# Kernel optimization log

Hardware: AMD Instinct MI355X
Metric: run time of the kernel (lower is better)

Reference implementation:

```python
import jax, jax.numpy as jnp
import numpy as np

SEQ_LEN = 8192
D_K = 128
NEG_BIG = 1000000000.0


def setup_inputs() -> dict:
    key = jax.random.key(0)
    kq, kk, kv = jax.random.split(key, 3)
    q = jax.random.normal(kq, (SEQ_LEN, D_K), dtype=jnp.float32)
    k = jax.random.normal(kk, (SEQ_LEN, D_K), dtype=jnp.float32)
    v = jax.random.normal(kv, (SEQ_LEN, D_K), dtype=jnp.float32)
    return {"q": q, "k": k, "v": v}


def reference(q, k, v):
    # q,k,v: (S, d). Naive attention with causal (look-ahead) mask, masked=True.
    d_k = q.shape[-1]
    scaled_logits = jnp.matmul(q, k.T) / jnp.sqrt(jnp.asarray(d_k, q.dtype))  # (S, S)
    look_ahead_mask = jnp.triu(jnp.ones((SEQ_LEN, SEQ_LEN), dtype=q.dtype), k=1)
    scaled_logits = scaled_logits - look_ahead_mask * NEG_BIG
    attn = jnp.matmul(jax.nn.softmax(scaled_logits, axis=-1), v)  # (S, d)
    return attn
```

## Files before the change

kernel.cpp:

```cpp
#include <hip/hip_runtime.h>
#include <hip/hip_bf16.h>
#include <math.h>

#define S_LEN 8192
#define DK    128
#define BM    128
#define BN    64
#define NQT   (S_LEN / BM)
#define SCALE2 (0.08838834764831845f * 1.4426950408889634f)

typedef __bf16 bf16x8_t __attribute__((ext_vector_type(8)));
typedef __bf16 bf16x4_t __attribute__((ext_vector_type(4)));
typedef __bf16 bf16x2_t __attribute__((ext_vector_type(2)));
typedef float  floatx16 __attribute__((ext_vector_type(16)));
typedef unsigned uintx4 __attribute__((ext_vector_type(4)));

#define GLD16(g, l) __builtin_amdgcn_global_load_lds(                      \
    (const __attribute__((address_space(1))) void*)(g),                    \
    (__attribute__((address_space(3))) void*)(l), 16, 0, 0)

__device__ __forceinline__ float fexp2(float x) {
#if __has_builtin(__builtin_amdgcn_exp2f)
  return __builtin_amdgcn_exp2f(x);
#else
  return exp2f(x);
#endif
}

__device__ __forceinline__ unsigned pack2(float a, float b) {
  bf16x2_t w; w[0] = (__bf16)a; w[1] = (__bf16)b;
  return __builtin_bit_cast(unsigned, w);
}

__device__ __forceinline__ void xswap(unsigned &x, unsigned &y) {
#if __has_builtin(__builtin_amdgcn_permlane32_swap)
  typedef unsigned v2u __attribute__((ext_vector_type(2)));
  v2u t = __builtin_amdgcn_permlane32_swap(x, y, false, false);
  x = t[0]; y = t[1];
#else
  const unsigned sx = (unsigned)__shfl_xor((int)x, 32);
  const unsigned sy = (unsigned)__shfl_xor((int)y, 32);
  const bool lo = ((threadIdx.x & 63) < 32);
  const unsigned nx = lo ? x : sy;
  const unsigned ny = lo ? sx : y;
  x = nx; y = ny;
#endif
}

__global__ __launch_bounds__(256) void prep_kv(const float* __restrict__ K,
                                               const float* __restrict__ V,
                                               __bf16* __restrict__ Kb,
                                               __bf16* __restrict__ Vt) {
  __shared__ __bf16 t[64][DK + 8];
  const int bx  = blockIdx.x;
  const int tid = threadIdx.x;
  if (bx < (S_LEN * DK) / (256 * 4)) {
    const int i = (bx * 256 + tid) * 4;
    float4 v = *(const float4*)&K[i];
    bf16x4_t b;
    b[0] = (__bf16)v.x; b[1] = (__bf16)v.y; b[2] = (__bf16)v.z; b[3] = (__bf16)v.w;
    *(bf16x4_t*)&Kb[i] = b;
    return;
  }
  const int key0 = (bx - (S_LEN * DK) / (256 * 4)) * 64;
  {
    const int r = tid >> 2, cg = (tid & 3) * 32;
    const float* vp = V + (size_t)(key0 + r) * DK + cg;
    #pragma unroll
    for (int i = 0; i < 8; ++i) {
      float4 v = ((const float4*)vp)[i];
      bf16x4_t b;
      b[0] = (__bf16)v.x; b[1] = (__bf16)v.y; b[2] = (__bf16)v.z; b[3] = (__bf16)v.w;
      *(bf16x4_t*)&t[r][cg + i * 4] = b;
    }
  }
  __syncthreads();
  const int d = tid >> 1, h = (tid & 1) * 32;
  __bf16* op = Vt + (size_t)d * S_LEN + key0 + h;
  #pragma unroll
  for (int jb = 0; jb < 4; ++jb) {
    bf16x8_t b;
    #pragma unroll
    for (int j = 0; j < 8; ++j) b[j] = t[h + jb * 8 + j][d];
    *(bf16x8_t*)&op[jb * 8] = b;
  }
}

__global__ __launch_bounds__(256, 2)
void fa_part(const float* __restrict__ Q, const __bf16* __restrict__ Kb,
             const __bf16* __restrict__ Vtg, float* __restrict__ Opart,
             float* __restrict__ stats, int C, int direct) {
  __shared__ __align__(16) __bf16 Ks[2][BN * DK];
  __shared__ __align__(16) __bf16 Vts[2][DK * BN];

  const int tid  = threadIdx.x;
  const int wave = tid >> 6;
  const int lane = tid & 63;
  const int l31  = lane & 31;
  const int hh   = lane >> 5;

  const int qtile = (NQT - 1) - blockIdx.x;
  const int g     = blockIdx.y;
  const int nt    = 2 * qtile + 2;
  const int jb0   = g * C;
  if (jb0 >= nt) return;
  const int jb1 = (jb0 + C < nt) ? (jb0 + C) : nt;
  const int h2 = C >> 1;
  const int ca = qtile / h2, cr = qtile - ca * h2;
  const int chunk = h2 * ca * (ca + 1) / 2 + cr * (ca + 1) + g;

  const int qw  = qtile * BM + wave * 32;
  const int myq = qw + l31;

  bf16x8_t qf[8];
  {
    const float* qrow = Q + (size_t)myq * DK + hh * 8;
    #pragma unroll
    for (int s = 0; s < 8; ++s) {
      float4 x = *(const float4*)(qrow + s * 16);
      float4 y = *(const float4*)(qrow + s * 16 + 4);
      bf16x8_t f;
      f[0]=(__bf16)(x.x*SCALE2); f[1]=(__bf16)(x.y*SCALE2);
      f[2]=(__bf16)(x.z*SCALE2); f[3]=(__bf16)(x.w*SCALE2);
      f[4]=(__bf16)(y.x*SCALE2); f[5]=(__bf16)(y.y*SCALE2);
      f[6]=(__bf16)(y.z*SCALE2); f[7]=(__bf16)(y.w*SCALE2);
      qf[s] = f;
    }
  }

  const __bf16* kp[4]; const __bf16* vp[4]; int loff[4];
  {
    const int ck = (lane & 15) ^ ((wave * 4 + (lane >> 4)) & 15);
    const int cv = (lane & 7) ^ ((lane >> 3) & 7);
    #pragma unroll
    for (int t = 0; t < 4; ++t) {
      const int rk = t * 16 + wave * 4 + (lane >> 4);
      kp[t] = Kb + ((size_t)(jb0 * BN + rk)) * DK + ck * 8;
      const int rv = t * 32 + wave * 8 + (lane >> 3);
      vp[t] = Vtg + (size_t)rv * S_LEN + jb0 * BN + cv * 8;
      loff[t] = t * 2048 + wave * 512;
    }
  }

  floatx16 o_acc[4];
  #pragma unroll
  for (int d = 0; d < 4; ++d)
    #pragma unroll
    for (int r = 0; r < 16; ++r) o_acc[d][r] = 0.f;
  float m_r = -INFINITY, l_r = 0.f;

  #pragma unroll
  for (int t = 0; t < 4; ++t) { GLD16(kp[t], &Ks[0][loff[t]]); kp[t] += BN * DK; }
  #pragma unroll
  for (int t = 0; t < 4; ++t) { GLD16(vp[t], &Vts[0][loff[t]]); vp[t] += BN; }
  __syncthreads();

  int cur = 0;
  for (int jb = jb0; jb < jb1; ++jb) {
    if (jb + 1 < jb1) {
      #pragma unroll
      for (int t = 0; t < 4; ++t) { GLD16(kp[t], &Ks[cur ^ 1][loff[t]]); kp[t] += BN * DK; }
      #pragma unroll
      for (int t = 0; t < 4; ++t) { GLD16(vp[t], &Vts[cur ^ 1][loff[t]]); vp[t] += BN; }
    }

    if (jb * 64 <= qw + 31) {
      const __bf16* Kc = Ks[cur];
      const __bf16* Vc = Vts[cur];

      floatx16 sv[2];
      __builtin_amdgcn_s_setprio(1);
      #pragma unroll
      for (int g1 = 0; g1 < 2; ++g1) {
        floatx16 acc;
        #pragma unroll
        for (int r = 0; r < 16; ++r) acc[r] = 0.f;
        const int row = g1 * 32 + l31;
        #pragma unroll
        for (int s = 0; s < 8; ++s) {
          bf16x8_t kf = *(const bf16x8_t*)
              &Kc[row * DK + (((s * 2 + hh) ^ (row & 15)) * 8)];
          acc = __builtin_amdgcn_mfma_f32_32x32x16_bf16(kf, qf[s], acc, 0, 0, 0);
        }
        sv[g1] = acc;
      }
      __builtin_amdgcn_s_setprio(0);

      if (jb * 64 + 63 > qw) {
        #pragma unroll
        for (int g1 = 0; g1 < 2; ++g1)
          #pragma unroll
          for (int r = 0; r < 16; ++r) {
            const int key = jb * 64 + g1 * 32 + (r & 3) + ((r >> 2) << 3) + (hh << 2);
            if (key > myq) sv[g1][r] = -1e30f;
          }
      }

      float pm = sv[0][0];
      #pragma unroll
      for (int g1 = 0; g1 < 2; ++g1)
        #pragma unroll
        for (int r = 0; r < 16; ++r) pm = fmaxf(pm, sv[g1][r]);
      {
        unsigned b0 = __builtin_bit_cast(unsigned, pm), b1 = b0;
        xswap(b0, b1);
        pm = fmaxf(__builtin_bit_cast(float, b0), __builtin_bit_cast(float, b1));
      }
      const int grow = (pm > m_r) ? 1 : 0;
      if (__any(grow)) {
        const float mn = fmaxf(m_r, pm);
        const float al = fexp2(m_r - mn);
        m_r = mn; l_r *= al;
        #pragma unroll
        for (int d = 0; d < 4; ++d)
          #pragma unroll
          for (int r = 0; r < 16; ++r) o_acc[d][r] *= al;
      }

      float rs = 0.f;
      #pragma unroll
      for (int g1 = 0; g1 < 2; ++g1)
        #pragma unroll
        for (int r = 0; r < 16; ++r) {
          const float pv = fexp2(sv[g1][r] - m_r);
          sv[g1][r] = pv;
          rs += pv;
        }
      {
        unsigned b0 = __builtin_bit_cast(unsigned, rs), b1 = b0;
        xswap(b0, b1);
        l_r += __builtin_bit_cast(float, b0) + __builtin_bit_cast(float, b1);
      }

      unsigned pk[4][4];
      #pragma unroll
      for (int g1 = 0; g1 < 2; ++g1) {
        unsigned W0 = pack2(sv[g1][0],  sv[g1][1]);
        unsigned W1 = pack2(sv[g1][2],  sv[g1][3]);
        unsigned W2 = pack2(sv[g1][4],  sv[g1][5]);
        unsigned W3 = pack2(sv[g1][6],  sv[g1][7]);
        unsigned W4 = pack2(sv[g1][8],  sv[g1][9]);
        unsigned W5 = pack2(sv[g1][10], sv[g1][11]);
        unsigned W6 = pack2(sv[g1][12], sv[g1][13]);
        unsigned W7 = pack2(sv[g1][14], sv[g1][15]);
        xswap(W0, W2); xswap(W1, W3);
        xswap(W4, W6); xswap(W5, W7);
        pk[g1*2+0][0]=W0; pk[g1*2+0][1]=W1; pk[g1*2+0][2]=W2; pk[g1*2+0][3]=W3;
        pk[g1*2+1][0]=W4; pk[g1*2+1][1]=W5; pk[g1*2+1][2]=W6; pk[g1*2+1][3]=W7;
      }

      __builtin_amdgcn_s_setprio(1);
      #pragma unroll
      for (int ks = 0; ks < 4; ++ks) {
        uintx4 u; u[0]=pk[ks][0]; u[1]=pk[ks][1]; u[2]=pk[ks][2]; u[3]=pk[ks][3];
        const bf16x8_t pf = __builtin_bit_cast(bf16x8_t, u);
        #pragma unroll
        for (int d = 0; d < 4; ++d) {
          const int row = d * 32 + l31;
          bf16x8_t vf = *(const bf16x8_t*)
              &Vc[row * BN + (((ks * 2 + hh) ^ (row & 7)) * 8)];
          o_acc[d] = __builtin_amdgcn_mfma_f32_32x32x16_bf16(vf, pf, o_acc[d], 0, 0, 0);
        }
      }
      __builtin_amdgcn_s_setprio(0);
    }

    __syncthreads();
    cur ^= 1;
  }

  if (direct) {
    const float inv = 1.0f / l_r;
    float* orow = Opart + (size_t)myq * DK;
    #pragma unroll
    for (int d = 0; d < 4; ++d)
      #pragma unroll
      for (int mI = 0; mI < 4; ++mI) {
        float4 st;
        st.x = o_acc[d][mI*4+0] * inv; st.y = o_acc[d][mI*4+1] * inv;
        st.z = o_acc[d][mI*4+2] * inv; st.w = o_acc[d][mI*4+3] * inv;
        *(float4*)&orow[d * 32 + mI * 8 + hh * 4] = st;
      }
  } else {
    float* orow = Opart + ((size_t)chunk * BM + wave * 32 + l31) * DK;
    #pragma unroll
    for (int d = 0; d < 4; ++d)
      #pragma unroll
      for (int mI = 0; mI < 4; ++mI) {
        float4 st;
        st.x = o_acc[d][mI*4+0]; st.y = o_acc[d][mI*4+1];
        st.z = o_acc[d][mI*4+2]; st.w = o_acc[d][mI*4+3];
        *(float4*)&orow[d * 32 + mI * 8 + hh * 4] = st;
      }
    if (hh == 0) {
      stats[((size_t)chunk * BM + wave * 32 + l31) * 2 + 0] = m_r;
      stats[((size_t)chunk * BM + wave * 32 + l31) * 2 + 1] = l_r;
    }
  }
}

__global__ __launch_bounds__(256)
void fa_reduce(const float* __restrict__ Opart, const float* __restrict__ stats,
               float* __restrict__ O, int C) {
  const int wave = threadIdx.x >> 6, lane = threadIdx.x & 63;
  const int row = blockIdx.x * 4 + wave;
  const int qt = row >> 7, r = row & 127;

  const int h2 = C >> 1;
  const int ca = qt / h2, cr = qt - ca * h2;
  const int base = h2 * ca * (ca + 1) / 2 + cr * (ca + 1);
  const int nch = (qt + h2) / h2;

  float M = -INFINITY;
  for (int g = 0; g < nch; ++g)
    M = fmaxf(M, stats[((size_t)(base + g) * BM + r) * 2]);

  float L = 0.f, ax = 0.f, ay = 0.f;
  for (int g = 0; g < nch; ++g) {
    const size_t sidx = (size_t)(base + g) * BM + r;
    const float m = stats[sidx * 2];
    const float w = fexp2(m - M);
    L += stats[sidx * 2 + 1] * w;
    float2 o = *(const float2*)&Opart[sidx * DK + lane * 2];
    ax += w * o.x; ay += w * o.y;
  }
  const float inv = 1.f / L;
  float2 res; res.x = ax * inv; res.y = ay * inv;
  *(float2*)&O[(size_t)row * DK + lane * 2] = res;
}

extern "C" void kernel_launch(void* const* d_in, const int* in_sizes, int n_in,
                              void* d_out, int out_size, void* d_ws, size_t ws_size,
                              hipStream_t stream) {
  (void)in_sizes; (void)n_in; (void)out_size;
  const float* q = (const float*)d_in[0];
  const float* k = (const float*)d_in[1];
  const float* v = (const float*)d_in[2];
  float* out = (float*)d_out;

  const size_t conv_bytes = (size_t)S_LEN * DK * 2 * 2;
  const size_t per_chunk  = (size_t)(BM * DK + 2 * BM) * 4;

  int C = 0; long long nc = 0;
  for (int c = 8; c <= 2 * NQT; c += 2) {
    const int h2 = c / 2;
    const int a = NQT / h2, rr = NQT - a * h2;
    const long long n = (long long)h2 * a * (a + 1) / 2 + (long long)rr * (a + 1);
    if (conv_bytes + (size_t)n * per_chunk <= ws_size) { C = c; nc = n; break; }
  }

  __bf16* Kb = (__bf16*)d_ws;
  __bf16* Vt = Kb + (size_t)S_LEN * DK;

  prep_kv<<<(S_LEN * DK) / (256 * 4) + S_LEN / 64, 256, 0, stream>>>(k, v, Kb, Vt);

  if (C) {
    float* Opart = (float*)(Vt + (size_t)S_LEN * DK);
    float* stats = Opart + (size_t)nc * BM * DK;
    const int gy = (2 * NQT + C - 1) / C;
    fa_part<<<dim3(NQT, gy), 256, 0, stream>>>(q, Kb, Vt, Opart, stats, C, 0);
    fa_reduce<<<S_LEN / 4, 256, 0, stream>>>(Opart, stats, out, C);
  } else {
    fa_part<<<dim3(NQT, 1), 256, 0, stream>>>(q, Kb, Vt, out, out, 2 * NQT, 1);
  }
}
```

Measured before the change: 124.2 us.

## Write single-chunk tiles directly, store fp16 normalized partials, defer rescale

Result: no change. 124.5 us (+0.2%).

```diff
diff --git a/kernel.cpp b/kernel.cpp
--- a/kernel.cpp
+++ b/kernel.cpp
@@ -8,12 +8,16 @@
 #define BN    64
 #define NQT   (S_LEN / BM)
 #define SCALE2 (0.08838834764831845f * 1.4426950408889634f)
+#define DEFER_THR 5.0f
 
 typedef __bf16 bf16x8_t __attribute__((ext_vector_type(8)));
 typedef __bf16 bf16x4_t __attribute__((ext_vector_type(4)));
 typedef __bf16 bf16x2_t __attribute__((ext_vector_type(2)));
 typedef float  floatx16 __attribute__((ext_vector_type(16)));
 typedef unsigned uintx4 __attribute__((ext_vector_type(4)));
+typedef _Float16 half_t;
+typedef _Float16 halfx4 __attribute__((ext_vector_type(4)));
+typedef _Float16 halfx2 __attribute__((ext_vector_type(2)));
 
 #define GLD16(g, l) __builtin_amdgcn_global_load_lds(                      \
     (const __attribute__((address_space(1))) void*)(g),                    \
@@ -88,8 +92,8 @@
 
 __global__ __launch_bounds__(256, 2)
 void fa_part(const float* __restrict__ Q, const __bf16* __restrict__ Kb,
-             const __bf16* __restrict__ Vtg, float* __restrict__ Opart,
-             float* __restrict__ stats, int C, int direct) {
+             const __bf16* __restrict__ Vtg, float* __restrict__ Out,
+             half_t* __restrict__ Opart, float* __restrict__ stats, int C) {
   __shared__ __align__(16) __bf16 Ks[2][BN * DK];
   __shared__ __align__(16) __bf16 Vts[2][DK * BN];
 
@@ -105,9 +109,11 @@
   const int jb0   = g * C;
   if (jb0 >= nt) return;
   const int jb1 = (jb0 + C < nt) ? (jb0 + C) : nt;
+
   const int h2 = C >> 1;
+  const int direct = (qtile < h2);
   const int ca = qtile / h2, cr = qtile - ca * h2;
-  const int chunk = h2 * ca * (ca + 1) / 2 + cr * (ca + 1) + g;
+  const int chunk = h2 * ca * (ca + 1) / 2 + cr * (ca + 1) - h2 + g;
 
   const int qw  = qtile * BM + wave * 32;
   const int myq = qw + l31;
@@ -196,18 +202,23 @@
           }
       }
 
-      float pm = sv[0][0];
-      #pragma unroll
-      for (int g1 = 0; g1 < 2; ++g1)
-        #pragma unroll
-        for (int r = 0; r < 16; ++r) pm = fmaxf(pm, sv[g1][r]);
+      float pmx[4];
+      #pragma unroll
+      for (int i = 0; i < 4; ++i)
+        pmx[i] = fmaxf(fmaxf(sv[0][i], sv[0][i + 4]),
+                       fmaxf(sv[0][i + 8], sv[0][i + 12]));
+      #pragma unroll
+      for (int i = 0; i < 4; ++i)
+        pmx[i] = fmaxf(pmx[i], fmaxf(fmaxf(sv[1][i], sv[1][i + 4]),
+                                     fmaxf(sv[1][i + 8], sv[1][i + 12])));
+      float pm = fmaxf(fmaxf(pmx[0], pmx[1]), fmaxf(pmx[2], pmx[3]));
       {
         unsigned b0 = __builtin_bit_cast(unsigned, pm), b1 = b0;
         xswap(b0, b1);
         pm = fmaxf(__builtin_bit_cast(float, b0), __builtin_bit_cast(float, b1));
       }
-      const int grow = (pm > m_r) ? 1 : 0;
-      if (__any(grow)) {
+
+      if (__any(pm > m_r + DEFER_THR)) {
         const float mn = fmaxf(m_r, pm);
         const float al = fexp2(m_r - mn);
         m_r = mn; l_r *= al;
@@ -217,15 +228,16 @@
           for (int r = 0; r < 16; ++r) o_acc[d][r] *= al;
       }
 
-      float rs = 0.f;
+      float rsx[4] = {0.f, 0.f, 0.f, 0.f};
       #pragma unroll
       for (int g1 = 0; g1 < 2; ++g1)
         #pragma unroll
         for (int r = 0; r < 16; ++r) {
           const float pv = fexp2(sv[g1][r] - m_r);
           sv[g1][r] = pv;
-          rs += pv;
+          rsx[r & 3] += pv;
         }
+      float rs = (rsx[0] + rsx[1]) + (rsx[2] + rsx[3]);
       {
         unsigned b0 = __builtin_bit_cast(unsigned, rs), b1 = b0;
         xswap(b0, b1);
@@ -270,8 +282,8 @@
   }
 
   if (direct) {
-    const float inv = 1.0f / l_r;
-    float* orow = Opart + (size_t)myq * DK;
+    const float inv = (l_r > 0.f) ? (1.0f / l_r) : 0.f;
+    float* orow = Out + (size_t)myq * DK;
     #pragma unroll
     for (int d = 0; d < 4; ++d)
       #pragma unroll
@@ -282,15 +294,18 @@
         *(float4*)&orow[d * 32 + mI * 8 + hh * 4] = st;
       }
   } else {
-    float* orow = Opart + ((size_t)chunk * BM + wave * 32 + l31) * DK;
+    const float inv = (l_r > 0.f) ? (1.0f / l_r) : 0.f;
+    half_t* orow = Opart + ((size_t)chunk * BM + wave * 32 + l31) * DK;
     #pragma unroll
     for (int d = 0; d < 4; ++d)
       #pragma unroll
       for (int mI = 0; mI < 4; ++mI) {
-        float4 st;
-        st.x = o_acc[d][mI*4+0]; st.y = o_acc[d][mI*4+1];
-        st.z = o_acc[d][mI*4+2]; st.w = o_acc[d][mI*4+3];
-        *(float4*)&orow[d * 32 + mI * 8 + hh * 4] = st;
+        halfx4 st;
+        st[0] = (half_t)(o_acc[d][mI*4+0] * inv);
+        st[1] = (half_t)(o_acc[d][mI*4+1] * inv);
+        st[2] = (half_t)(o_acc[d][mI*4+2] * inv);
+        st[3] = (half_t)(o_acc[d][mI*4+3] * inv);
+        *(halfx4*)&orow[d * 32 + mI * 8 + hh * 4] = st;
       }
     if (hh == 0) {
       stats[((size_t)chunk * BM + wave * 32 + l31) * 2 + 0] = m_r;
@@ -300,15 +315,15 @@
 }
 
 __global__ __launch_bounds__(256)
-void fa_reduce(const float* __restrict__ Opart, const float* __restrict__ stats,
+void fa_reduce(const half_t* __restrict__ Opart, const float* __restrict__ stats,
                float* __restrict__ O, int C) {
+  const int h2 = C >> 1;
   const int wave = threadIdx.x >> 6, lane = threadIdx.x & 63;
-  const int row = blockIdx.x * 4 + wave;
+  const int row = h2 * BM + blockIdx.x * 4 + wave;
   const int qt = row >> 7, r = row & 127;
 
-  const int h2 = C >> 1;
-  const int ca = qt / h2, cr = qt - ca * h2;
-  const int base = h2 * ca * (ca + 1) / 2 + cr * (ca + 1);
+  const int a = qt / h2, rr = qt - a * h2;
+  const int base = h2 * a * (a + 1) / 2 + rr * (a + 1) - h2;
   const int nch = (qt + h2) / h2;
 
   float M = -INFINITY;
@@ -319,10 +334,10 @@
   for (int g = 0; g < nch; ++g) {
     const size_t sidx = (size_t)(base + g) * BM + r;
     const float m = stats[sidx * 2];
-    const float w = fexp2(m - M);
-    L += stats[sidx * 2 + 1] * w;
-    float2 o = *(const float2*)&Opart[sidx * DK + lane * 2];
-    ax += w * o.x; ay += w * o.y;
+    const float wl = fexp2(m - M) * stats[sidx * 2 + 1];
+    L += wl;
+    halfx2 o = *(const halfx2*)&Opart[sidx * DK + lane * 2];
+    ax += wl * (float)o[0]; ay += wl * (float)o[1];
   }
   const float inv = 1.f / L;
   float2 res; res.x = ax * inv; res.y = ay * inv;
@@ -339,28 +354,30 @@
   float* out = (float*)d_out;
 
   const size_t conv_bytes = (size_t)S_LEN * DK * 2 * 2;
-  const size_t per_chunk  = (size_t)(BM * DK + 2 * BM) * 4;
-
-  int C = 0; long long nc = 0;
-  for (int c = 8; c <= 2 * NQT; c += 2) {
-    const int h2 = c / 2;
-    const int a = NQT / h2, rr = NQT - a * h2;
-    const long long n = (long long)h2 * a * (a + 1) / 2 + (long long)rr * (a + 1);
+  const size_t per_chunk  = (size_t)BM * DK * 2 + 2 * BM * 4;
+
+  int C = 2 * NQT; long long nc = 0;
+  for (int c = 8; c < 2 * NQT; c += 2) {
+    const int hh2 = c / 2;
+    const int a = NQT / hh2, rr = NQT - a * hh2;
+    const long long F64 = (long long)hh2 * a * (a + 1) / 2 + (long long)rr * (a + 1);
+    const long long n = F64 - hh2;
     if (conv_bytes + (size_t)n * per_chunk <= ws_size) { C = c; nc = n; break; }
   }
 
   __bf16* Kb = (__bf16*)d_ws;
   __bf16* Vt = Kb + (size_t)S_LEN * DK;
+  half_t* Opart = (half_t*)(Vt + (size_t)S_LEN * DK);
+  float* stats = (float*)(Opart + (size_t)nc * BM * DK);
 
   prep_kv<<<(S_LEN * DK) / (256 * 4) + S_LEN / 64, 256, 0, stream>>>(k, v, Kb, Vt);
 
-  if (C) {
-    float* Opart = (float*)(Vt + (size_t)S_LEN * DK);
-    float* stats = Opart + (size_t)nc * BM * DK;
-    const int gy = (2 * NQT + C - 1) / C;
-    fa_part<<<dim3(NQT, gy), 256, 0, stream>>>(q, Kb, Vt, Opart, stats, C, 0);
-    fa_reduce<<<S_LEN / 4, 256, 0, stream>>>(Opart, stats, out, C);
-  } else {
-    fa_part<<<dim3(NQT, 1), 256, 0, stream>>>(q, Kb, Vt, out, out, 2 * NQT, 1);
-  }
-}
+  const int gy = (2 * NQT + C - 1) / C;
+  fa_part<<<dim3(NQT, gy), 256, 0, stream>>>(q, Kb, Vt, out, Opart, stats, C);
+
+  if (nc > 0) {
+    const int h2 = C / 2;
+    const int nrows = (NQT - h2) * BM;
+    fa_reduce<<<nrows / 4, 256, 0, stream>>>(Opart, stats, out, C);
+  }
+}
```
